# Performance work log

Measured on AMD Instinct MI355X. Metric: run time of the kernel, lower is better.

Reference implementation:

```python
import jax, jax.numpy as jnp
import numpy as np

NUM_KNOTS = 64
HEAD_DIM = 4
SCALE = 0.5  # 1/sqrt(4)


def setup_inputs() -> dict:
    key = jax.random.key(0)
    ks = jax.random.split(key, 6)
    B, L, D = 4, 128, 256
    s = 1.0 / np.sqrt(D)
    return {
        "x": jax.random.normal(ks[0], (B, L, D), dtype=jnp.float32),
        "Wq": jax.random.normal(ks[1], (D, D), dtype=jnp.float32) * s,
        "Wk": jax.random.normal(ks[2], (D, D), dtype=jnp.float32) * s,
        "Wv": jax.random.normal(ks[3], (D, D), dtype=jnp.float32) * s,
        "Wo": jax.random.normal(ks[4], (D, D), dtype=jnp.float32) * s,
        "bo": jnp.zeros((D,), dtype=jnp.float32),
    }


def reference(x, Wq, Wk, Wv, Wo, bo):
    # x: [B, L, D], D = NUM_KNOTS * HEAD_DIM = 256
    B, L, D = x.shape
    N = L * NUM_KNOTS  # flattened 'knot' sequence length
    # nn.Linear applies x @ W.T
    q = (x @ Wq.T).reshape(B, N, HEAD_DIM)
    k = (x @ Wk.T).reshape(B, N, HEAD_DIM)
    v = (x @ Wv.T).reshape(B, N, HEAD_DIM)
    # full attention over the length-N knot sequence (head_dim = 4)
    logits = jnp.einsum("bnd,bmd->bnm", q, k) * SCALE  # [B, N, N]
    attn = jax.nn.softmax(logits, axis=-1)
    out = jnp.einsum("bnm,bmd->bnd", attn, v).reshape(B, L, D)
    return out @ Wo.T + bo
```

## Files before the change

kernel.cpp:

```cpp
#include <hip/hip_runtime.h>
#include <stdint.h>

#define NQ 8192
#define DIM 256
#define KSPLIT 8

#define QSCALE 0.7213475204444817f

typedef _Float16 half8  __attribute__((ext_vector_type(8)));
typedef float    f32x16 __attribute__((ext_vector_type(16)));

union H8 { uint32_t u[4]; half8 h; };

__device__ __forceinline__ float ex2(float x) { return __builtin_amdgcn_exp2f(x); }
__device__ __forceinline__ uint32_t pkrtz(float a, float b) {
    auto h = __builtin_amdgcn_cvt_pkrtz(a, b);
    return __builtin_bit_cast(uint32_t, h);
}

__global__ __launch_bounds__(256) void qkv_proj(
    const float* __restrict__ x,
    const float* __restrict__ Wq, const float* __restrict__ Wk,
    const float* __restrict__ Wv,
    _Float16* __restrict__ Qh, _Float16* __restrict__ Kh,
    _Float16* __restrict__ Vthi, _Float16* __restrict__ Vtlo)
{
    const int m = blockIdx.y;
    const float* W = (m == 0) ? Wq : (m == 1) ? Wk : Wv;
    const int j  = threadIdx.x;
    const int rb = blockIdx.x * 4;

    float acc[4] = {0.f, 0.f, 0.f, 0.f};
    const float4* __restrict__ W4 = reinterpret_cast<const float4*>(W + j * DIM);
    const float*  __restrict__ A0 = x + rb * DIM;

    #pragma unroll 4
    for (int d4 = 0; d4 < DIM / 4; ++d4) {
        const float4 w = W4[d4];
        #pragma unroll
        for (int r = 0; r < 4; ++r) {
            const float4 a = reinterpret_cast<const float4*>(A0 + r * DIM)[d4];
            acc[r] = fmaf(a.x, w.x, acc[r]);
            acc[r] = fmaf(a.y, w.y, acc[r]);
            acc[r] = fmaf(a.z, w.z, acc[r]);
            acc[r] = fmaf(a.w, w.w, acc[r]);
        }
    }
    #pragma unroll
    for (int r = 0; r < 4; ++r) {
        const int rr = rb + r;
        const int bb = rr >> 7, rowin = rr & 127;
        const int n = rowin * 64 + (j >> 2), comp = j & 3;
        if (m == 2) {
            const _Float16 hi = (_Float16)acc[r];
            const _Float16 lo = (_Float16)(acc[r] - (float)hi);
            Vthi[((size_t)bb * 4 + comp) * NQ + n] = hi;
            Vtlo[((size_t)bb * 4 + comp) * NQ + n] = lo;
        } else {
            const float v = (m == 0) ? acc[r] * QSCALE : acc[r];
            const _Float16 hi = (_Float16)v;
            const _Float16 lo = (_Float16)(v - (float)hi);
            _Float16* dst = ((m == 0) ? Qh : Kh) + ((size_t)bb * NQ + n) * 8 + comp;
            dst[0] = hi;
            dst[4] = lo;
        }
    }
}

__global__ __launch_bounds__(256) void attn_mfma(
    const _Float16* __restrict__ Qh, const _Float16* __restrict__ Kh,
    const _Float16* __restrict__ Vthi, const _Float16* __restrict__ Vtlo,
    float* __restrict__ Pp)
{
    const int t    = threadIdx.x;
    const int w    = t >> 6;
    const int lane = t & 63;
    const int lo   = lane & 31, hi = lane >> 5;
    const int qstrip = blockIdx.x * 4 + w;
    const int ks     = blockIdx.y;
    const int b      = blockIdx.z;
    const int qbase  = qstrip * 32;
    const int kbase  = ks * 1024;

    H8 qhi, qlo;
    {
        uint4 qd = make_uint4(0, 0, 0, 0);
        if (lane < 32)
            qd = *reinterpret_cast<const uint4*>(Qh + ((size_t)b * NQ + qbase + lo) * 8);
        qhi.u[0] = qd.x; qhi.u[1] = qd.y;
        qhi.u[2] = (lane < 32) ? 0x00003C00u : 0u;
        qhi.u[3] = 0;
        qlo.u[0] = qd.z; qlo.u[1] = qd.w; qlo.u[2] = 0; qlo.u[3] = 0;
    }
    const _Float16* __restrict__ KhB = Kh + (size_t)b * NQ * 8;
    const int c = lo;
    const _Float16* __restrict__ VrowH = Vthi + ((size_t)b * 4 + (c < 4 ? c : 0)) * NQ;
    const _Float16* __restrict__ VrowL = Vtlo + ((size_t)b * 4 + (c < 4 ? c : 0)) * NQ;

    f32x16 acc = {};

    auto LDK = [&](int kt) -> uint4 {
        return (lane < 32)
            ? *reinterpret_cast<const uint4*>(KhB + (size_t)(kt + lo) * 8)
            : make_uint4(0, 0, 0, 0);
    };
    auto LDVH = [&](int kt) -> uint4 {
        if (c < 4)  return *reinterpret_cast<const uint4*>(VrowH + kt + hi * 8);
        if (c == 4) return make_uint4(0x3C003C00u, 0x3C003C00u, 0x3C003C00u, 0x3C003C00u);
        return make_uint4(0, 0, 0, 0);
    };
    auto LDVL = [&](int kt) -> uint4 {
        if (c < 4) return *reinterpret_cast<const uint4*>(VrowL + kt + hi * 8);
        return make_uint4(0, 0, 0, 0);
    };

    uint4 kd  = LDK(kbase);
    uint4 v1h = LDVH(kbase),      v1l = LDVL(kbase);
    uint4 v2h = LDVH(kbase + 16), v2l = LDVL(kbase + 16);

    #pragma unroll 1
    for (int tt = 0; tt < 32; ++tt) {
        uint4 kdn = kd, v1hn = v1h, v1ln = v1l, v2hn = v2h, v2ln = v2l;
        if (tt < 31) {
            const int kt2 = kbase + (tt + 1) * 32;
            kdn = LDK(kt2);
            v1hn = LDVH(kt2);      v1ln = LDVL(kt2);
            v2hn = LDVH(kt2 + 16); v2ln = LDVL(kt2 + 16);
        }

        H8 ahi, alo;
        ahi.u[0] = kd.x; ahi.u[1] = kd.y;
        ahi.u[2] = (lane < 32) ? 0x0000C900u : 0u;
        ahi.u[3] = 0;
        alo.u[0] = kd.z; alo.u[1] = kd.w; alo.u[2] = 0; alo.u[3] = 0;
        f32x16 z = {};
        f32x16 S = __builtin_amdgcn_mfma_f32_32x32x16_f16(ahi.h, qhi.h, z, 0, 0, 0);
        S = __builtin_amdgcn_mfma_f32_32x32x16_f16(ahi.h, qlo.h, S, 0, 0, 0);
        S = __builtin_amdgcn_mfma_f32_32x32x16_f16(alo.h, qhi.h, S, 0, 0, 0);

        float p[16];
        #pragma unroll
        for (int g = 0; g < 16; ++g) p[g] = ex2(S[g]);

        uint32_t u0 = pkrtz(p[0], p[1]), u1 = pkrtz(p[2], p[3]);
        uint32_t u2 = pkrtz(p[4], p[5]), u3 = pkrtz(p[6], p[7]);
        asm("v_permlane32_swap_b32 %0, %1" : "+v"(u0), "+v"(u2));
        asm("v_permlane32_swap_b32 %0, %1" : "+v"(u1), "+v"(u3));
        H8 pf1; pf1.u[0] = u0; pf1.u[1] = u1; pf1.u[2] = u2; pf1.u[3] = u3;
        H8 vf;
        vf.u[0] = v1h.x; vf.u[1] = v1h.y; vf.u[2] = v1h.z; vf.u[3] = v1h.w;
        acc = __builtin_amdgcn_mfma_f32_32x32x16_f16(vf.h, pf1.h, acc, 0, 0, 0);
        vf.u[0] = v1l.x; vf.u[1] = v1l.y; vf.u[2] = v1l.z; vf.u[3] = v1l.w;
        acc = __builtin_amdgcn_mfma_f32_32x32x16_f16(vf.h, pf1.h, acc, 0, 0, 0);

        uint32_t u4 = pkrtz(p[8], p[9]),   u5 = pkrtz(p[10], p[11]);
        uint32_t u6 = pkrtz(p[12], p[13]), u7 = pkrtz(p[14], p[15]);
        asm("v_permlane32_swap_b32 %0, %1" : "+v"(u4), "+v"(u6));
        asm("v_permlane32_swap_b32 %0, %1" : "+v"(u5), "+v"(u7));
        H8 pf2; pf2.u[0] = u4; pf2.u[1] = u5; pf2.u[2] = u6; pf2.u[3] = u7;
        vf.u[0] = v2h.x; vf.u[1] = v2h.y; vf.u[2] = v2h.z; vf.u[3] = v2h.w;
        acc = __builtin_amdgcn_mfma_f32_32x32x16_f16(vf.h, pf2.h, acc, 0, 0, 0);
        vf.u[0] = v2l.x; vf.u[1] = v2l.y; vf.u[2] = v2l.z; vf.u[3] = v2l.w;
        acc = __builtin_amdgcn_mfma_f32_32x32x16_f16(vf.h, pf2.h, acc, 0, 0, 0);

        kd = kdn; v1h = v1hn; v1l = v1ln; v2h = v2hn; v2l = v2ln;
    }

    float* __restrict__ Pb = Pp + (((size_t)(b * KSPLIT + ks)) * NQ + qbase) * 8;
    if (lane < 32) {
        *reinterpret_cast<float4*>(Pb + lo * 8) =
            make_float4(acc[0], acc[1], acc[2], acc[3]);
    } else {
        Pb[lo * 8 + 4] = acc[0];
    }
}

__global__ __launch_bounds__(256) void merge_oproj(
    const float* __restrict__ Pp, const float* __restrict__ Wo,
    const float* __restrict__ bo, float* __restrict__ out)
{
    __shared__ float aoL[4][DIM];

    const int rb = blockIdx.x * 4;
    const int b  = rb >> 7;
    const int n0 = (rb & 127) * 64;
    const int t  = threadIdx.x;

    {
        const int n = n0 + t;
        float4 num = make_float4(0.f, 0.f, 0.f, 0.f);
        float den = 0.f;
        #pragma unroll
        for (int s = 0; s < KSPLIT; ++s) {
            const float* q = Pp + (((size_t)(b * KSPLIT + s)) * NQ + n) * 8;
            const float4 v4 = *reinterpret_cast<const float4*>(q);
            num.x += v4.x; num.y += v4.y; num.z += v4.z; num.w += v4.w;
            den += q[4];
        }
        const float inv = 1.0f / den;
        const int row = t >> 6;
        const int d0  = (t & 63) * 4;
        aoL[row][d0 + 0] = num.x * inv;
        aoL[row][d0 + 1] = num.y * inv;
        aoL[row][d0 + 2] = num.z * inv;
        aoL[row][d0 + 3] = num.w * inv;
    }
    __syncthreads();

    const int j = t;
    float acc[4] = {0.f, 0.f, 0.f, 0.f};
    const float4* __restrict__ W4 = reinterpret_cast<const float4*>(Wo + j * DIM);
    #pragma unroll 4
    for (int d4 = 0; d4 < DIM / 4; ++d4) {
        const float4 wv = W4[d4];
        #pragma unroll
        for (int r = 0; r < 4; ++r) {
            const float4 a = reinterpret_cast<const float4*>(&aoL[r][0])[d4];
            acc[r] = fmaf(a.x, wv.x, acc[r]);
            acc[r] = fmaf(a.y, wv.y, acc[r]);
            acc[r] = fmaf(a.z, wv.z, acc[r]);
            acc[r] = fmaf(a.w, wv.w, acc[r]);
        }
    }
    const float bias = bo[j];
    #pragma unroll
    for (int r = 0; r < 4; ++r)
        out[(rb + r) * DIM + j] = acc[r] + bias;
}

extern "C" void kernel_launch(void* const* d_in, const int* in_sizes, int n_in,
                              void* d_out, int out_size, void* d_ws, size_t ws_size,
                              hipStream_t stream) {
    const float* x  = (const float*)d_in[0];
    const float* Wq = (const float*)d_in[1];
    const float* Wk = (const float*)d_in[2];
    const float* Wv = (const float*)d_in[3];
    const float* Wo = (const float*)d_in[4];
    const float* bo = (const float*)d_in[5];
    float* out = (float*)d_out;

    _Float16* Qh   = (_Float16*)d_ws;
    _Float16* Kh   = Qh + 4 * NQ * 8;
    _Float16* Vthi = Kh + 4 * NQ * 8;
    _Float16* Vtlo = Vthi + 4 * 4 * NQ;
    float*    Pp   = (float*)(Vtlo + 4 * 4 * NQ);

    qkv_proj<<<dim3(128, 3), 256, 0, stream>>>(x, Wq, Wk, Wv, Qh, Kh, Vthi, Vtlo);
    attn_mfma<<<dim3(64, KSPLIT, 4), 256, 0, stream>>>(Qh, Kh, Vthi, Vtlo, Pp);
    merge_oproj<<<128, 256, 0, stream>>>(Pp, Wo, bo, out);
}
```

Before: 102.2 us.

## Pack split-precision Q/K/V operands to cut MFMAs per attention tile

The Q/K hi/lo split terms and the softmax offset are repacked into a two-half layout, so a single 32x32x16 MFMA computes the split-precision logits instead of three. V hi and lo are stacked as separate rows of one packed operand, with a row of ones for the softmax denominator, so P·V needs one MFMA per 16 keys instead of two. The hi and lo halves of the output are summed with a lane swap after the loop, and the loop is unrolled by 2. This removes most of the MFMA and register-shuffling work in the inner loop. In exchange the workspace layout is larger, and unused V rows are left uninitialized but ignored.

```diff
diff --git a/kernel.cpp b/kernel.cpp
--- a/kernel.cpp
+++ b/kernel.cpp
@@ -10,7 +10,7 @@
 typedef _Float16 half8  __attribute__((ext_vector_type(8)));
 typedef float    f32x16 __attribute__((ext_vector_type(16)));
 
-union H8 { uint32_t u[4]; half8 h; };
+union H8 { uint32_t u[4]; uint4 u4; half8 h; };
 
 __device__ __forceinline__ float ex2(float x) { return __builtin_amdgcn_exp2f(x); }
 __device__ __forceinline__ uint32_t pkrtz(float a, float b) {
@@ -22,8 +22,8 @@
     const float* __restrict__ x,
     const float* __restrict__ Wq, const float* __restrict__ Wk,
     const float* __restrict__ Wv,
-    _Float16* __restrict__ Qh, _Float16* __restrict__ Kh,
-    _Float16* __restrict__ Vthi, _Float16* __restrict__ Vtlo)
+    _Float16* __restrict__ Qpack, _Float16* __restrict__ Kpack,
+    _Float16* __restrict__ Vpack)
 {
     const int m = blockIdx.y;
     const float* W = (m == 0) ? Wq : (m == 1) ? Wk : Wv;
@@ -54,89 +54,75 @@
         if (m == 2) {
             const _Float16 hi = (_Float16)acc[r];
             const _Float16 lo = (_Float16)(acc[r] - (float)hi);
-            Vthi[((size_t)bb * 4 + comp) * NQ + n] = hi;
-            Vtlo[((size_t)bb * 4 + comp) * NQ + n] = lo;
+            Vpack[((size_t)bb * 32 + comp) * NQ + n]     = hi;
+            Vpack[((size_t)bb * 32 + 4 + comp) * NQ + n] = lo;
+            if (comp == 0)
+                Vpack[((size_t)bb * 32 + 8) * NQ + n] = (_Float16)1.0f;
         } else {
             const float v = (m == 0) ? acc[r] * QSCALE : acc[r];
             const _Float16 hi = (_Float16)v;
             const _Float16 lo = (_Float16)(v - (float)hi);
-            _Float16* dst = ((m == 0) ? Qh : Kh) + ((size_t)bb * NQ + n) * 8 + comp;
-            dst[0] = hi;
-            dst[4] = lo;
+            _Float16* pk = (m == 0) ? Qpack : Kpack;
+            _Float16* d0 = pk + (((size_t)bb * 2 + 0) * NQ + n) * 8;
+            _Float16* d1 = pk + (((size_t)bb * 2 + 1) * NQ + n) * 8;
+            if (m == 0) {
+                d0[comp] = hi; d0[4 + comp] = lo;
+                d1[comp] = hi;
+                d1[4 + comp] = (comp == 0) ? (_Float16)1.0f : (_Float16)0.0f;
+            } else {
+                d0[comp] = hi; d0[4 + comp] = hi;
+                d1[comp] = lo;
+                d1[4 + comp] = (comp == 0) ? (_Float16)(-10.0f) : (_Float16)0.0f;
+            }
         }
     }
 }
 
 __global__ __launch_bounds__(256) void attn_mfma(
-    const _Float16* __restrict__ Qh, const _Float16* __restrict__ Kh,
-    const _Float16* __restrict__ Vthi, const _Float16* __restrict__ Vtlo,
-    float* __restrict__ Pp)
+    const _Float16* __restrict__ Qpack, const _Float16* __restrict__ Kpack,
+    const _Float16* __restrict__ Vpack, float* __restrict__ Pp)
 {
     const int t    = threadIdx.x;
     const int w    = t >> 6;
     const int lane = t & 63;
-    const int lo   = lane & 31, hi = lane >> 5;
+    const int l5   = lane & 31, h1 = lane >> 5;
     const int qstrip = blockIdx.x * 4 + w;
     const int ks     = blockIdx.y;
     const int b      = blockIdx.z;
     const int qbase  = qstrip * 32;
     const int kbase  = ks * 1024;
 
-    H8 qhi, qlo;
-    {
-        uint4 qd = make_uint4(0, 0, 0, 0);
-        if (lane < 32)
-            qd = *reinterpret_cast<const uint4*>(Qh + ((size_t)b * NQ + qbase + lo) * 8);
-        qhi.u[0] = qd.x; qhi.u[1] = qd.y;
-        qhi.u[2] = (lane < 32) ? 0x00003C00u : 0u;
-        qhi.u[3] = 0;
-        qlo.u[0] = qd.z; qlo.u[1] = qd.w; qlo.u[2] = 0; qlo.u[3] = 0;
-    }
-    const _Float16* __restrict__ KhB = Kh + (size_t)b * NQ * 8;
-    const int c = lo;
-    const _Float16* __restrict__ VrowH = Vthi + ((size_t)b * 4 + (c < 4 ? c : 0)) * NQ;
-    const _Float16* __restrict__ VrowL = Vtlo + ((size_t)b * 4 + (c < 4 ? c : 0)) * NQ;
+    H8 qf;
+    qf.u4 = *reinterpret_cast<const uint4*>(
+        Qpack + (((size_t)b * 2 + h1) * NQ + qbase + l5) * 8);
+
+    const _Float16* __restrict__ Kb_ = Kpack + ((size_t)b * 2 + h1) * NQ * 8;
+    const _Float16* __restrict__ Vb_ = Vpack + ((size_t)b * 32 + l5) * NQ + h1 * 8;
 
     f32x16 acc = {};
 
     auto LDK = [&](int kt) -> uint4 {
-        return (lane < 32)
-            ? *reinterpret_cast<const uint4*>(KhB + (size_t)(kt + lo) * 8)
-            : make_uint4(0, 0, 0, 0);
+        return *reinterpret_cast<const uint4*>(Kb_ + (size_t)(kt + l5) * 8);
     };
-    auto LDVH = [&](int kt) -> uint4 {
-        if (c < 4)  return *reinterpret_cast<const uint4*>(VrowH + kt + hi * 8);
-        if (c == 4) return make_uint4(0x3C003C00u, 0x3C003C00u, 0x3C003C00u, 0x3C003C00u);
-        return make_uint4(0, 0, 0, 0);
+    auto LDV = [&](int kt) -> uint4 {
+        return *reinterpret_cast<const uint4*>(Vb_ + kt);
     };
-    auto LDVL = [&](int kt) -> uint4 {
-        if (c < 4) return *reinterpret_cast<const uint4*>(VrowL + kt + hi * 8);
-        return make_uint4(0, 0, 0, 0);
-    };
-
-    uint4 kd  = LDK(kbase);
-    uint4 v1h = LDVH(kbase),      v1l = LDVL(kbase);
-    uint4 v2h = LDVH(kbase + 16), v2l = LDVL(kbase + 16);
-
-    #pragma unroll 1
+
+    uint4 kd = LDK(kbase);
+    uint4 v1 = LDV(kbase);
+    uint4 v2 = LDV(kbase + 16);
+
+    #pragma unroll 2
     for (int tt = 0; tt < 32; ++tt) {
-        uint4 kdn = kd, v1hn = v1h, v1ln = v1l, v2hn = v2h, v2ln = v2l;
+        uint4 kdn = kd, v1n = v1, v2n = v2;
         if (tt < 31) {
             const int kt2 = kbase + (tt + 1) * 32;
-            kdn = LDK(kt2);
-            v1hn = LDVH(kt2);      v1ln = LDVL(kt2);
-            v2hn = LDVH(kt2 + 16); v2ln = LDVL(kt2 + 16);
-        }
-
-        H8 ahi, alo;
-        ahi.u[0] = kd.x; ahi.u[1] = kd.y;
-        ahi.u[2] = (lane < 32) ? 0x0000C900u : 0u;
-        ahi.u[3] = 0;
-        alo.u[0] = kd.z; alo.u[1] = kd.w; alo.u[2] = 0; alo.u[3] = 0;
+            kdn = LDK(kt2); v1n = LDV(kt2); v2n = LDV(kt2 + 16);
+        }
+
+        H8 af; af.u4 = kd;
         f32x16 z = {};
-        f32x16 S = __builtin_amdgcn_mfma_f32_32x32x16_f16(ahi.h, qhi.h, z, 0, 0, 0);
-        S = __builtin_amdgcn_mfma_f32_32x32x16_f16(ahi.h, qlo.h, S, 0, 0, 0);
-        S = __builtin_amdgcn_mfma_f32_32x32x16_f16(alo.h, qhi.h, S, 0, 0, 0);
+        f32x16 S = __builtin_amdgcn_mfma_f32_32x32x16_f16(af.h, qf.h, z, 0, 0, 0);
 
         float p[16];
         #pragma unroll
@@ -147,31 +133,33 @@
         asm("v_permlane32_swap_b32 %0, %1" : "+v"(u0), "+v"(u2));
         asm("v_permlane32_swap_b32 %0, %1" : "+v"(u1), "+v"(u3));
         H8 pf1; pf1.u[0] = u0; pf1.u[1] = u1; pf1.u[2] = u2; pf1.u[3] = u3;
-        H8 vf;
-        vf.u[0] = v1h.x; vf.u[1] = v1h.y; vf.u[2] = v1h.z; vf.u[3] = v1h.w;
-        acc = __builtin_amdgcn_mfma_f32_32x32x16_f16(vf.h, pf1.h, acc, 0, 0, 0);
-        vf.u[0] = v1l.x; vf.u[1] = v1l.y; vf.u[2] = v1l.z; vf.u[3] = v1l.w;
-        acc = __builtin_amdgcn_mfma_f32_32x32x16_f16(vf.h, pf1.h, acc, 0, 0, 0);
+        H8 vf1; vf1.u4 = v1;
+        acc = __builtin_amdgcn_mfma_f32_32x32x16_f16(vf1.h, pf1.h, acc, 0, 0, 0);
 
         uint32_t u4 = pkrtz(p[8], p[9]),   u5 = pkrtz(p[10], p[11]);
         uint32_t u6 = pkrtz(p[12], p[13]), u7 = pkrtz(p[14], p[15]);
         asm("v_permlane32_swap_b32 %0, %1" : "+v"(u4), "+v"(u6));
         asm("v_permlane32_swap_b32 %0, %1" : "+v"(u5), "+v"(u7));
         H8 pf2; pf2.u[0] = u4; pf2.u[1] = u5; pf2.u[2] = u6; pf2.u[3] = u7;
-        vf.u[0] = v2h.x; vf.u[1] = v2h.y; vf.u[2] = v2h.z; vf.u[3] = v2h.w;
-        acc = __builtin_amdgcn_mfma_f32_32x32x16_f16(vf.h, pf2.h, acc, 0, 0, 0);
-        vf.u[0] = v2l.x; vf.u[1] = v2l.y; vf.u[2] = v2l.z; vf.u[3] = v2l.w;
-        acc = __builtin_amdgcn_mfma_f32_32x32x16_f16(vf.h, pf2.h, acc, 0, 0, 0);
-
-        kd = kdn; v1h = v1hn; v1l = v1ln; v2h = v2hn; v2l = v2ln;
-    }
+        H8 vf2; vf2.u4 = v2;
+        acc = __builtin_amdgcn_mfma_f32_32x32x16_f16(vf2.h, pf2.h, acc, 0, 0, 0);
+
+        kd = kdn; v1 = v1n; v2 = v2n;
+    }
+
+    float n0 = acc[0], n1 = acc[1], n2 = acc[2], n3 = acc[3];
+    const float ls = acc[4];
+    float t0 = 0.f, t1 = 0.f, t2 = 0.f, t3 = 0.f;
+    asm("v_permlane32_swap_b32 %0, %1" : "+v"(n0), "+v"(t0));
+    asm("v_permlane32_swap_b32 %0, %1" : "+v"(n1), "+v"(t1));
+    asm("v_permlane32_swap_b32 %0, %1" : "+v"(n2), "+v"(t2));
+    asm("v_permlane32_swap_b32 %0, %1" : "+v"(n3), "+v"(t3));
+    n0 += t0; n1 += t1; n2 += t2; n3 += t3;
 
     float* __restrict__ Pb = Pp + (((size_t)(b * KSPLIT + ks)) * NQ + qbase) * 8;
     if (lane < 32) {
-        *reinterpret_cast<float4*>(Pb + lo * 8) =
-            make_float4(acc[0], acc[1], acc[2], acc[3]);
-    } else {
-        Pb[lo * 8 + 4] = acc[0];
+        *reinterpret_cast<float4*>(Pb + l5 * 8) = make_float4(n0, n1, n2, n3);
+        Pb[l5 * 8 + 4] = ls;
     }
 }
 
@@ -239,13 +227,12 @@
     const float* bo = (const float*)d_in[5];
     float* out = (float*)d_out;
 
-    _Float16* Qh   = (_Float16*)d_ws;
-    _Float16* Kh   = Qh + 4 * NQ * 8;
-    _Float16* Vthi = Kh + 4 * NQ * 8;
-    _Float16* Vtlo = Vthi + 4 * 4 * NQ;
-    float*    Pp   = (float*)(Vtlo + 4 * 4 * NQ);
-
-    qkv_proj<<<dim3(128, 3), 256, 0, stream>>>(x, Wq, Wk, Wv, Qh, Kh, Vthi, Vtlo);
-    attn_mfma<<<dim3(64, KSPLIT, 4), 256, 0, stream>>>(Qh, Kh, Vthi, Vtlo, Pp);
+    _Float16* Qpack = (_Float16*)d_ws;
+    _Float16* Kpack = Qpack + 4 * 2 * NQ * 8;
+    _Float16* Vpack = Kpack + 4 * 2 * NQ * 8;
+    float*    Pp    = (float*)(Vpack + 4 * 32 * NQ);
+
+    qkv_proj<<<dim3(128, 3), 256, 0, stream>>>(x, Wq, Wk, Wv, Qpack, Kpack, Vpack);
+    attn_mfma<<<dim3(64, KSPLIT, 4), 256, 0, stream>>>(Qpack, Kpack, Vpack, Pp);
     merge_oproj<<<128, 256, 0, stream>>>(Pp, Wo, bo, out);
 }
```

Result: faster. 100.0 us (-2.1%).
